# Kernel tuning notes

Measured on AMD Instinct MI355X. Metric: run time of the kernel, lower is better.

The kernel has to match this reference:

```python
import jax, jax.numpy as jnp
import numpy as np

B, P, G, E = 2, 16, 128, 96
C110, C011, C001 = 4, 2, 1
N, CO = 128, 2

def _pw(x, W, b):
    """1x1 conv of any spatial rank == pointwise channel mixing."""
    y = jnp.einsum('oc,bc...->bo...', W, x)
    return y + b.reshape((1, -1) + (1,) * (y.ndim - 2))

def _hidden(s110, s011, s001, Ws, bs):
    # s110:[B,C,P,G,1]  s011:[B,C,1,G,E]  s001:[B,C,1,1,E]
    # sub-stream order: [110 full, 110 pool-P, 110 pool-G, 011 full, 011 pool-G, 011 pool-E, 001]
    t110 = s110[..., 0]         # [B,C,P,G]
    t011 = s011[:, :, 0]        # [B,C,G,E]
    t001 = s001[:, :, 0, 0]     # [B,C,E]
    s = (_pw(t110, Ws[0], bs[0])[..., None]
         + _pw(t110.max(axis=2), Ws[1], bs[1])[:, :, None, :, None]
         + _pw(t110.max(axis=3), Ws[2], bs[2])[:, :, :, None, None]
         + _pw(t011, Ws[3], bs[3])[:, :, None, :, :]
         + _pw(t011.max(axis=2), Ws[4], bs[4])[:, :, None, None, :]
         + _pw(t011.max(axis=3), Ws[5], bs[5])[:, :, None, :, None]
         + _pw(t001, Ws[6], bs[6])[:, :, None, None, :])
    s = jax.nn.leaky_relu(s)    # [B,N,P,G,E]
    return (jnp.max(s, axis=4, keepdims=True),
            jnp.max(s, axis=2, keepdims=True),
            jnp.max(s, axis=(2, 3), keepdims=True))

def _forward(x110, x011, x001, W0_110, b0_110, W0_011, b0_011, W0_001, b0_001, W1, b1, Wact, bact, Wcrit, bcrit):
    Ws0 = [W0_110[0], W0_110[1], W0_110[2], W0_011[0], W0_011[1], W0_011[2], W0_001]
    bs0 = [b0_110[0], b0_110[1], b0_110[2], b0_011[0], b0_011[1], b0_011[2], b0_001]
    s110, s011, s001 = _hidden(x110, x011, x001, Ws0, bs0)
    s110, s011, s001 = _hidden(s110, s011, s001, list(W1), list(b1))
    t110 = s110[..., 0]  # [B,N,P,G]
    # actor head: eliminate G,E via mean pooling (dim_elimination_max_pooling=False)
    a110 = _pw(t110.mean(axis=3), Wact[0], bact[0])              # [B,CO,P]
    a011 = _pw(s011.mean(axis=(3, 4)), Wact[1], bact[1])         # [B,CO,1]
    a001 = _pw(s001[:, :, :, 0].mean(axis=3), Wact[2], bact[2])  # [B,CO,1]
    actions = jax.nn.leaky_relu(a110 + a011 + a001)              # [B,CO,P]
    # critic head: eliminate G via mean pooling
    c110 = _pw(t110.mean(axis=3), Wcrit[0], bcrit[0])            # [B,CO,P]
    c011 = _pw(s011[:, :, 0].mean(axis=2), Wcrit[1], bcrit[1])   # [B,CO,E]
    c001 = _pw(s001[:, :, 0, 0], Wcrit[2], bcrit[2])             # [B,CO,E]
    v = jax.nn.leaky_relu(c110[:, :, :, None] + (c011 + c001)[:, :, None, :])  # [B,CO,P,E]
    v110 = v.max(axis=3).sum(axis=2)  # stream (1,1,0): max over E, sum over P
    v011 = v.max(axis=2).sum(axis=2)  # streams (0,1,1) and (0,0,1) coincide numerically
    values = (2.0 + v110 + 2.0 * v011).reshape(-1)  # python sum(l, 2) starts at 2
    return actions, values

def setup_inputs() -> dict:
    key = jax.random.key(0)
    ks = jax.random.split(key, 12)
    f32 = jnp.float32
    def w(k, shape, fan):
        return jax.random.normal(k, shape, f32) / np.float32(np.sqrt(fan))
    return {
        'x110': jax.random.normal(ks[0], (B, C110, P, G, 1), f32),
        'x011': jax.random.normal(ks[1], (B, C011, 1, G, E), f32),
        'x001': jax.random.normal(ks[2], (B, C001, 1, 1, E), f32),
        'W0_110': w(ks[3], (3, N, C110), C110), 'b0_110': jnp.zeros((3, N), f32),
        'W0_011': w(ks[4], (3, N, C011), C011), 'b0_011': jnp.zeros((3, N), f32),
        'W0_001': w(ks[5], (N, C001), C001),    'b0_001': jnp.zeros((N,), f32),
        'W1':     w(ks[6], (7, N, N), N),       'b1':     jnp.zeros((7, N), f32),
        'Wact':   w(ks[7], (3, CO, N), N),      'bact':   jnp.zeros((3, CO), f32),
        'Wcrit':  w(ks[8], (3, CO, N), N),      'bcrit':  jnp.zeros((3, CO), f32),
    }

def reference(x110, x011, x001, W0_110, b0_110, W0_011, b0_011, W0_001, b0_001, W1, b1, Wact, bact, Wcrit, bcrit):
    return _forward(x110, x011, x001, W0_110, b0_110, W0_011, b0_011, W0_001, b0_001, W1, b1, Wact, bact, Wcrit, bcrit)
```

## Files before the change

### kernel.cpp

```cpp
#include <hip/hip_runtime.h>
#include <math.h>

#define DEVI __device__ __forceinline__

constexpr int B = 2, P = 16, G = 128, E = 96, N = 128, CO = 2;

DEVI float lrelu(float x) { return x > 0.f ? x : 0.01f * x; }

constexpr int OFF_U1     = 0;
constexpr int OFF_V1     = OFF_U1 + 524288;
constexpr int OFF_MAXPU0 = OFF_V1 + 3145728;
constexpr int OFF_MAXEV0 = OFF_MAXPU0 + 32768;
constexpr int OFF_MP110  = OFF_MAXEV0 + 32768;
constexpr int OFF_MG110  = OFF_MP110 + 32768;
constexpr int OFF_S001A  = OFF_MG110 + 4096;
constexpr int OFF_RMP    = OFF_S001A + 24576;
constexpr int OFF_RMG    = OFF_RMP + 1024;
constexpr int OFF_RME    = OFF_RMG + 128;
constexpr int OFF_RMG011 = OFF_RME + 512;
constexpr int OFF_C1P    = OFF_RMG011 + 384;
constexpr int OFF_BF1G   = OFF_C1P + 4096;
constexpr int OFF_EG1E   = OFF_BF1G + 32768;
constexpr int OFF_M110   = OFF_EG1E + 24576;
constexpr int OFF_M011E  = OFF_M110 + 4096;
constexpr int OFF_S001B  = OFF_M011E + 24576;

__global__ void __launch_bounds__(256) k_layer0(
    const float* __restrict__ x110, const float* __restrict__ x011,
    const float* __restrict__ x001,
    const float* __restrict__ W0_110, const float* __restrict__ b0_110,
    const float* __restrict__ W0_011, const float* __restrict__ b0_011,
    const float* __restrict__ W0_001, const float* __restrict__ b0_001,
    float* __restrict__ maxpU0g, float* __restrict__ maxeV0g,
    float* __restrict__ mp110, float* __restrict__ mg110,
    float* __restrict__ s001a,
    float* __restrict__ rmpG, float* __restrict__ rmgG,
    float* __restrict__ rmeG, float* __restrict__ rmg011G) {
  __shared__ float xs[4 * 16 * 128];
  __shared__ float v0[128 * 97];
  __shared__ float u0[16 * 128];
  __shared__ float rmp[4 * 128], rmgS[4 * 16], rme[2 * 128], rmg011L[2 * 96];
  __shared__ float mpu[128], mev[128], part[256];
  const int bn = blockIdx.x, b = bn >> 7, n = bn & 127, tid = threadIdx.x;

  {
    const float4* xsrc = (const float4*)(x110 + (size_t)b * 8192);
    float4* xdst = (float4*)xs;
#pragma unroll
    for (int k = 0; k < 8; k++) xdst[tid + k * 256] = xsrc[tid + k * 256];
  }
  __syncthreads();
  for (int i = tid; i < 512; i += 256) {
    int c = i >> 7, g = i & 127;
    float m = -INFINITY;
    for (int p = 0; p < P; p++) m = fmaxf(m, xs[(c * 16 + p) * 128 + g]);
    rmp[i] = m;
  }
  if (tid < 64) {
    int c = tid >> 4, p = tid & 15;
    float m = -INFINITY;
    for (int g = 0; g < G; g++) m = fmaxf(m, xs[(c * 16 + p) * 128 + g]);
    rmgS[tid] = m;
  }
  {
    int c = tid >> 7, g = tid & 127;
    const float4* r = (const float4*)(x011 + ((size_t)(b * 2 + c) * 128 + g) * 96);
    float m = -INFINITY;
#pragma unroll
    for (int j = 0; j < 24; j++) {
      float4 v = r[j];
      m = fmaxf(m, fmaxf(fmaxf(v.x, v.y), fmaxf(v.z, v.w)));
    }
    rme[tid] = m;
  }
  if (tid < 192) {
    int c = tid / 96, e = tid % 96;
    const float* pp = x011 + ((size_t)(b * 2 + c) * 128) * 96 + e;
    float m = -INFINITY;
    for (int g = 0; g < G; g++) m = fmaxf(m, pp[g * 96]);
    rmg011L[tid] = m;
  }
  __syncthreads();
  float w0[4], w1[4], w2[4];
#pragma unroll
  for (int cc = 0; cc < 4; cc++) {
    w0[cc] = W0_110[n * 4 + cc];
    w1[cc] = W0_110[512 + n * 4 + cc];
    w2[cc] = W0_110[1024 + n * 4 + cc];
  }
  float we0 = W0_011[512 + n * 2], we1 = W0_011[512 + n * 2 + 1];
  float bu = b0_110[n] + b0_110[128 + n] + b0_110[256 + n] + b0_011[256 + n];
  float vw00 = W0_011[n * 2], vw01 = W0_011[n * 2 + 1];
  float vw10 = W0_011[256 + n * 2], vw11 = W0_011[256 + n * 2 + 1];
  float w001 = W0_001[n];
  float bv = b0_011[n] + b0_011[128 + n] + b0_001[n];

#pragma unroll
  for (int k = 0; k < 8; k++) {
    int i = tid + k * 256, p = i >> 7, g = i & 127;
    float acc = bu + we0 * rme[g] + we1 * rme[128 + g];
#pragma unroll
    for (int cc = 0; cc < 4; cc++)
      acc += w0[cc] * xs[(cc * 16 + p) * 128 + g] + w1[cc] * rmp[cc * 128 + g]
           + w2[cc] * rmgS[cc * 16 + p];
    u0[i] = acc;
  }
  {
    const float* xa = x011 + (size_t)(b * 2) * 12288;
    const float* xb = xa + 12288;
    const float* xc = x001 + b * 96;
    for (int k = 0; k < 48; k++) {
      int i = tid + k * 256;
      int g = i / 96, e = i - g * 96;
      float val = bv + vw00 * xa[i] + vw01 * xb[i]
                + vw10 * rmg011L[e] + vw11 * rmg011L[96 + e] + w001 * xc[e];
      v0[g * 97 + e] = val;
    }
  }
  __syncthreads();
  if (tid < 128) {
    float m = -INFINITY;
    for (int p = 0; p < P; p++) m = fmaxf(m, u0[p * 128 + tid]);
    mpu[tid] = m;
    maxpU0g[bn * 128 + tid] = m;
  }
  {
    int g = tid & 127, h = tid >> 7;
    const float* r = &v0[g * 97 + h * 48];
    float m = -INFINITY;
    for (int j = 0; j < 48; j++) m = fmaxf(m, r[j]);
    part[tid] = m;
  }
  __syncthreads();
  if (tid < 128) {
    float m = fmaxf(part[tid], part[128 + tid]);
    mev[tid] = m;
    maxeV0g[bn * 128 + tid] = m;
    mp110[bn * 128 + tid] = lrelu(mpu[tid] + m);
  }
  __syncthreads();
  {
    int p = tid >> 4, ch = tid & 15;
    float m = -INFINITY;
    for (int g = ch * 8; g < ch * 8 + 8; g++)
      m = fmaxf(m, u0[p * 128 + g] + mev[g]);
    part[tid] = m;
  }
  if (tid < 96) {
    float m = -INFINITY;
    for (int g = 0; g < G; g++) m = fmaxf(m, mpu[g] + v0[g * 97 + tid]);
    s001a[bn * 96 + tid] = lrelu(m);
  }
  __syncthreads();
  if (tid < 16) {
    float m = -INFINITY;
    for (int ch = 0; ch < 16; ch++) m = fmaxf(m, part[tid * 16 + ch]);
    mg110[bn * 16 + tid] = lrelu(m);
  }
  if (n == 0) {
    for (int i = tid; i < 512; i += 256) rmpG[b * 512 + i] = rmp[i];
    if (tid < 64) rmgG[b * 64 + tid] = rmgS[tid];
    rmeG[b * 256 + tid] = rme[tid];
    if (tid < 192) rmg011G[b * 192 + tid] = rmg011L[tid];
  }
}

__global__ void k_sg(const float* __restrict__ W1, const float* __restrict__ mp110,
                     const float* __restrict__ mg110, const float* __restrict__ s001a,
                     float* __restrict__ C1p, float* __restrict__ BF1g,
                     float* __restrict__ EG1e) {
  int t = blockIdx.x * 256 + threadIdx.x;
  if (t < 4096) {
    int p = t & 15, n = (t >> 4) & 127, b = t >> 11;
    float acc = 0.f;
    for (int c = 0; c < N; c++)
      acc += W1[(2 * N + n) * N + c] * mg110[(b * N + c) * P + p];
    C1p[t] = acc;
  } else if (t < 36864) {
    int i = t - 4096;
    int g = i & 127, n = (i >> 7) & 127, b = i >> 14;
    float acc = 0.f;
    for (int c = 0; c < N; c++)
      acc += (W1[(1 * N + n) * N + c] + W1[(5 * N + n) * N + c])
             * mp110[(b * N + c) * G + g];
    BF1g[i] = acc;
  } else {
    int i = t - 36864;
    int e = i % 96; int r = i / 96; int n = r & 127, b = r >> 7;
    float acc = 0.f;
    for (int c = 0; c < N; c++)
      acc += (W1[(4 * N + n) * N + c] + W1[(6 * N + n) * N + c])
             * s001a[(b * N + c) * E + e];
    EG1e[i] = acc;
  }
}

__global__ void __launch_bounds__(256) k_layer1(
    const float* __restrict__ x110, const float* __restrict__ x011,
    const float* __restrict__ x001,
    const float* __restrict__ W0_110, const float* __restrict__ b0_110,
    const float* __restrict__ W0_011, const float* __restrict__ b0_011,
    const float* __restrict__ W0_001, const float* __restrict__ b0_001,
    const float* __restrict__ maxpU0g, const float* __restrict__ maxeV0g,
    const float* __restrict__ rmpG, const float* __restrict__ rmgG,
    const float* __restrict__ rmeG, const float* __restrict__ rmg011G,
    const float* __restrict__ W1, const float* __restrict__ b1,
    const float* __restrict__ C1p, const float* __restrict__ BF1g,
    const float* __restrict__ EG1e,
    float* __restrict__ U1, float* __restrict__ V1) {
  __shared__ float s110c[128 * 16];
  __shared__ float s011c[128 * 96];
  __shared__ float W0L110[1536], W0L011[768], W0L001[128];
  __shared__ float busum[128], bvsum[128], mpu[128], mev[128];
  __shared__ float x011row[192], rmg011s[192], x001s[96];
  __shared__ float x110col[64], rmg110p[64], rmp4[4], rme2[2];
  const int blk = blockIdx.x;
  const int b = blk >> 8, g = (blk >> 1) & 127, nh = blk & 1;
  const int n0 = nh * 64;
  const int tid = threadIdx.x;

  for (int i = tid; i < 1536; i += 256) W0L110[i] = W0_110[i];
  for (int i = tid; i < 768; i += 256) W0L011[i] = W0_011[i];
  if (tid < 128) {
    W0L001[tid] = W0_001[tid];
    busum[tid] = b0_110[tid] + b0_110[128 + tid] + b0_110[256 + tid] + b0_011[256 + tid];
    bvsum[tid] = b0_011[tid] + b0_011[128 + tid] + b0_001[tid];
    mpu[tid] = maxpU0g[(b * 128 + tid) * 128 + g];
    mev[tid] = maxeV0g[(b * 128 + tid) * 128 + g];
  }
  if (tid < 192) {
    int c = tid / 96, e = tid % 96;
    x011row[tid] = x011[((size_t)(b * 2 + c) * 128 + g) * 96 + e];
    rmg011s[tid] = rmg011G[b * 192 + tid];
  }
  if (tid < 96) x001s[tid] = x001[b * 96 + tid];
  if (tid < 64) {
    int c = tid >> 4, p = tid & 15;
    x110col[tid] = x110[((size_t)(b * 4 + c) * 16 + p) * 128 + g];
    rmg110p[tid] = rmgG[b * 64 + tid];
  }
  if (tid < 4) rmp4[tid] = rmpG[(b * 4 + tid) * 128 + g];
  if (tid < 2) rme2[tid] = rmeG[(b * 2 + tid) * 128 + g];
  __syncthreads();

#pragma unroll
  for (int k = 0; k < 8; k++) {
    int i = tid + k * 256, c = i >> 4, p = i & 15;
    float acc = busum[c] + W0L011[512 + c * 2] * rme2[0]
              + W0L011[512 + c * 2 + 1] * rme2[1];
#pragma unroll
    for (int cc = 0; cc < 4; cc++)
      acc += W0L110[c * 4 + cc] * x110col[cc * 16 + p]
           + W0L110[512 + c * 4 + cc] * rmp4[cc]
           + W0L110[1024 + c * 4 + cc] * rmg110p[cc * 16 + p];
    s110c[i] = lrelu(acc + mev[c]);
  }
  for (int k = 0; k < 48; k++) {
    int i = tid + k * 256;
    int c = i / 96, e = i - c * 96;
    float v = bvsum[c] + W0L011[c * 2] * x011row[e] + W0L011[c * 2 + 1] * x011row[96 + e]
            + W0L011[256 + c * 2] * rmg011s[e] + W0L011[256 + c * 2 + 1] * rmg011s[96 + e]
            + W0L001[c] * x001s[e];
    s011c[i] = lrelu(v + mpu[c]);
  }
  __syncthreads();

  {
    int nn = tid >> 2, pq = tid & 3;
    int n = n0 + nn;
    float bb = b1[n] + b1[128 + n] + b1[256 + n] + b1[640 + n]
             + BF1g[(b * 128 + n) * 128 + g];
    float4 cp = *(const float4*)&C1p[(b * 128 + n) * 16 + pq * 4];
    float4 a = make_float4(bb + cp.x, bb + cp.y, bb + cp.z, bb + cp.w);
    const float* wr = W1 + (size_t)n * 128;
    for (int c = 0; c < 128; c++) {
      float wv = wr[c];
      float4 s = *(const float4*)&s110c[c * 16 + pq * 4];
      a.x += wv * s.x; a.y += wv * s.y; a.z += wv * s.z; a.w += wv * s.w;
    }
    float* dst = U1 + ((size_t)(b * 128 + n) * 16 + pq * 4) * 128 + g;
    dst[0] = a.x; dst[128] = a.y; dst[256] = a.z; dst[384] = a.w;
  }
  {
    int n2 = tid >> 3, e0 = (tid & 7) * 12;
    int na = n0 + n2 * 2, nb = na + 1;
    float4 aA[3], aB[3];
    {
      float bbA = b1[384 + na] + b1[512 + na] + b1[768 + na];
      float bbB = b1[384 + nb] + b1[512 + nb] + b1[768 + nb];
      const float* egA = EG1e + (b * 128 + na) * 96 + e0;
      const float* egB = EG1e + (b * 128 + nb) * 96 + e0;
#pragma unroll
      for (int k = 0; k < 3; k++) {
        aA[k] = make_float4(bbA + egA[k * 4], bbA + egA[k * 4 + 1],
                            bbA + egA[k * 4 + 2], bbA + egA[k * 4 + 3]);
        aB[k] = make_float4(bbB + egB[k * 4], bbB + egB[k * 4 + 1],
                            bbB + egB[k * 4 + 2], bbB + egB[k * 4 + 3]);
      }
    }
    const float* wA = W1 + (size_t)(384 + na) * 128;
    const float* wB = W1 + (size_t)(384 + nb) * 128;
#pragma unroll 4
    for (int c = 0; c < 128; c++) {
      float4 s0 = *(const float4*)&s011c[c * 96 + e0];
      float4 s1 = *(const float4*)&s011c[c * 96 + e0 + 4];
      float4 s2 = *(const float4*)&s011c[c * 96 + e0 + 8];
      float wa = wA[c], wb = wB[c];
      aA[0].x += wa * s0.x; aA[0].y += wa * s0.y; aA[0].z += wa * s0.z; aA[0].w += wa * s0.w;
      aA[1].x += wa * s1.x; aA[1].y += wa * s1.y; aA[1].z += wa * s1.z; aA[1].w += wa * s1.w;
      aA[2].x += wa * s2.x; aA[2].y += wa * s2.y; aA[2].z += wa * s2.z; aA[2].w += wa * s2.w;
      aB[0].x += wb * s0.x; aB[0].y += wb * s0.y; aB[0].z += wb * s0.z; aB[0].w += wb * s0.w;
      aB[1].x += wb * s1.x; aB[1].y += wb * s1.y; aB[1].z += wb * s1.z; aB[1].w += wb * s1.w;
      aB[2].x += wb * s2.x; aB[2].y += wb * s2.y; aB[2].z += wb * s2.z; aB[2].w += wb * s2.w;
    }
    float* dA = V1 + ((size_t)(b * 128 + na) * 128 + g) * 96 + e0;
    float* dB = V1 + ((size_t)(b * 128 + nb) * 128 + g) * 96 + e0;
#pragma unroll
    for (int k = 0; k < 3; k++) {
      *(float4*)(dA + k * 4) = aA[k];
      *(float4*)(dB + k * 4) = aB[k];
    }
  }
}

__global__ void __launch_bounds__(256) k_post1(
    const float* __restrict__ U1, const float* __restrict__ V1,
    float* __restrict__ m110, float* __restrict__ m011e,
    float* __restrict__ s001b) {
  __shared__ float uU[P * G];
  __shared__ float part[256];
  __shared__ float smaxeV[G], smaxpU[G];
  const int bn = blockIdx.x;
  const int tid = threadIdx.x;
  const float4* usrc = (const float4*)(U1 + (size_t)bn * P * G);
  float4* udst = (float4*)uU;
  udst[tid] = usrc[tid];
  udst[tid + 256] = usrc[tid + 256];
  {
    int g = tid & 127, h = tid >> 7;
    const float* vrow = V1 + ((size_t)bn * G + g) * E + h * 48;
    float m = -INFINITY;
#pragma unroll
    for (int j = 0; j < 12; j++) {
      float4 v = *(const float4*)(vrow + j * 4);
      m = fmaxf(m, fmaxf(fmaxf(v.x, v.y), fmaxf(v.z, v.w)));
    }
    part[tid] = m;
  }
  __syncthreads();
  if (tid < G) {
    smaxeV[tid] = fmaxf(part[tid], part[tid + 128]);
    float mp = -INFINITY;
    for (int p = 0; p < P; p++) mp = fmaxf(mp, uU[p * G + tid]);
    smaxpU[tid] = mp;
  }
  __syncthreads();
  if (tid < P) {
    float s = 0.f;
    for (int g = 0; g < G; g++) s += lrelu(uU[tid * G + g] + smaxeV[g]);
    m110[bn * P + tid] = s * (1.f / G);
  }
  if (tid < E) {
    float s = 0.f, mm = -INFINITY;
    const float* vcol = V1 + (size_t)bn * G * E + tid;
    for (int g = 0; g < G; g++) {
      float pre = smaxpU[g] + vcol[g * E];
      s += lrelu(pre);
      mm = fmaxf(mm, pre);
    }
    m011e[bn * E + tid] = s * (1.f / G);
    s001b[bn * E + tid] = lrelu(mm);
  }
}

__global__ void __launch_bounds__(128) k_final(const float* __restrict__ m110,
                                               const float* __restrict__ m011e,
                                               const float* __restrict__ s001,
                                               const float* __restrict__ Wact,
                                               const float* __restrict__ bact,
                                               const float* __restrict__ Wcrit,
                                               const float* __restrict__ bcrit,
                                               float* __restrict__ out) {
  __shared__ float sm011[N], sm001[N], scp[P], sce[E], srow[P], scol[E];
  const int bo = blockIdx.x;
  const int o = bo & 1, b = bo >> 1;
  const int t = threadIdx.x;
  {
    float s1 = 0.f, s2 = 0.f;
    const float* p1 = m011e + (b * N + t) * E;
    const float* p2 = s001 + (b * N + t) * E;
    for (int e = 0; e < E; e++) { s1 += p1[e]; s2 += p2[e]; }
    sm011[t] = s1 * (1.f / E);
    sm001[t] = s2 * (1.f / E);
  }
  __syncthreads();
  if (t < P) {
    const float* wa0 = Wact + o * N;
    const float* wa1 = Wact + (1 * CO + o) * N;
    const float* wa2 = Wact + (2 * CO + o) * N;
    const float* wc0 = Wcrit + o * N;
    float a = 0.f, c = 0.f, aa = 0.f;
    for (int n = 0; n < N; n++) {
      float m = m110[(b * N + n) * P + t];
      a += wa0[n] * m;
      c += wc0[n] * m;
      aa += wa1[n] * sm011[n] + wa2[n] * sm001[n];
    }
    float act = a + aa + bact[o] + bact[CO + o] + bact[2 * CO + o];
    out[(b * CO + o) * P + t] = lrelu(act);
    scp[t] = c + bcrit[o];
  } else if (t < P + E) {
    int e = t - P;
    const float* wc1 = Wcrit + (1 * CO + o) * N;
    const float* wc2 = Wcrit + (2 * CO + o) * N;
    float c = 0.f;
    for (int n = 0; n < N; n++)
      c += wc1[n] * m011e[(b * N + n) * E + e] + wc2[n] * s001[(b * N + n) * E + e];
    sce[e] = c + bcrit[CO + o] + bcrit[2 * CO + o];
  }
  __syncthreads();
  if (t < P) {
    float m = -INFINITY;
    for (int e = 0; e < E; e++) m = fmaxf(m, lrelu(scp[t] + sce[e]));
    srow[t] = m;
  } else if (t < P + E) {
    int e = t - P;
    float m = -INFINITY;
    for (int p = 0; p < P; p++) m = fmaxf(m, lrelu(scp[p] + sce[e]));
    scol[e] = m;
  }
  __syncthreads();
  if (t == 0) {
    float v110 = 0.f, v011 = 0.f;
    for (int p = 0; p < P; p++) v110 += srow[p];
    for (int e = 0; e < E; e++) v011 += scol[e];
    out[B * CO * P + b * CO + o] = 2.f + v110 + 2.f * v011;
  }
}

extern "C" void kernel_launch(void* const* d_in, const int* in_sizes, int n_in,
                              void* d_out, int out_size, void* d_ws, size_t ws_size,
                              hipStream_t stream) {
  const float* x110   = (const float*)d_in[0];
  const float* x011   = (const float*)d_in[1];
  const float* x001   = (const float*)d_in[2];
  const float* W0_110 = (const float*)d_in[3];
  const float* b0_110 = (const float*)d_in[4];
  const float* W0_011 = (const float*)d_in[5];
  const float* b0_011 = (const float*)d_in[6];
  const float* W0_001 = (const float*)d_in[7];
  const float* b0_001 = (const float*)d_in[8];
  const float* W1     = (const float*)d_in[9];
  const float* b1     = (const float*)d_in[10];
  const float* Wact   = (const float*)d_in[11];
  const float* bact   = (const float*)d_in[12];
  const float* Wcrit  = (const float*)d_in[13];
  const float* bcrit  = (const float*)d_in[14];
  float* out = (float*)d_out;
  float* w = (float*)d_ws;

  float* U1     = w + OFF_U1;
  float* V1     = w + OFF_V1;
  float* maxpU0 = w + OFF_MAXPU0;
  float* maxeV0 = w + OFF_MAXEV0;
  float* mp110  = w + OFF_MP110;
  float* mg110  = w + OFF_MG110;
  float* s001a  = w + OFF_S001A;
  float* rmpG   = w + OFF_RMP;
  float* rmgG   = w + OFF_RMG;
  float* rmeG   = w + OFF_RME;
  float* rmg011 = w + OFF_RMG011;
  float* C1p    = w + OFF_C1P;
  float* BF1g   = w + OFF_BF1G;
  float* EG1e   = w + OFF_EG1E;
  float* m110   = w + OFF_M110;
  float* m011e  = w + OFF_M011E;
  float* s001b  = w + OFF_S001B;

  k_layer0<<<256, 256, 0, stream>>>(x110, x011, x001, W0_110, b0_110, W0_011,
                                    b0_011, W0_001, b0_001,
                                    maxpU0, maxeV0, mp110, mg110, s001a,
                                    rmpG, rmgG, rmeG, rmg011);
  k_sg<<<240, 256, 0, stream>>>(W1, mp110, mg110, s001a, C1p, BF1g, EG1e);
  k_layer1<<<512, 256, 0, stream>>>(x110, x011, x001, W0_110, b0_110, W0_011,
                                    b0_011, W0_001, b0_001,
                                    maxpU0, maxeV0, rmpG, rmgG, rmeG, rmg011,
                                    W1, b1, C1p, BF1g, EG1e, U1, V1);
  k_post1<<<256, 256, 0, stream>>>(U1, V1, m110, m011e, s001b);
  k_final<<<4, 128, 0, stream>>>(m110, m011e, s001b, Wact, bact, Wcrit, bcrit, out);
}
```

Baseline: 104.7 us.

## Fuse all five stages into one persistent kernel with atomic grid barriers

Replaces the five separate kernel launches with a single 256-block persistent kernel. Stages are separated by software grid barriers built on atomic counters, and the counters are reset by a memset before each launch. Shared memory is shared between stages through a union. The layer-1 stage is remapped so each block handles one (b,g) pair instead of the previous 512-block split, and the post stage now stages V1 into shared memory. The aim is to remove launch gaps and inter-kernel drain, at the cost of spin-wait barriers, a larger shared-memory footprint that may lower occupancy, and reliance on all 256 blocks being co-resident.

```diff
diff --git a/kernel.cpp b/kernel.cpp
--- a/kernel.cpp
+++ b/kernel.cpp
@@ -4,6 +4,7 @@
 #define DEVI __device__ __forceinline__
 
 constexpr int B = 2, P = 16, G = 128, E = 96, N = 128, CO = 2;
+constexpr int NBLK = 256;
 
 DEVI float lrelu(float x) { return x > 0.f ? x : 0.01f * x; }
 
@@ -24,417 +25,459 @@
 constexpr int OFF_M110   = OFF_EG1E + 24576;
 constexpr int OFF_M011E  = OFF_M110 + 4096;
 constexpr int OFF_S001B  = OFF_M011E + 24576;
-
-__global__ void __launch_bounds__(256) k_layer0(
+constexpr int OFF_CTR    = OFF_S001B + 24576;
+
+union alignas(16) SharedU {
+  struct {
+    float xs[4 * 16 * 128];
+    float v0[128 * 97];
+    float u0[16 * 128];
+    float rmp[512], rmgS[64], rme[256], rmg011L[192];
+    float mpu[128], mev[128], part[256];
+  } a;
+  struct {
+    float s110c[128 * 16];
+    float s011c[128 * 96];
+    float W0L110[1536], W0L011[768], W0L001[128];
+    float busum[128], bvsum[128], mpu[128], mev[128];
+    float x011row[192], rmg011s[192], x001s[96];
+    float x110col[64], rmg110p[64], rmp4[4], rme2[2];
+  } c;
+  struct {
+    float vrow[128 * 97];
+    float uU[16 * 128];
+    float part[256];
+    float smaxeV[128], smaxpU[128];
+  } d;
+  struct {
+    float sm011[128], sm001[128], scp[16], sce[96], srow[16], scol[96];
+  } e;
+};
+
+DEVI void grid_sync(unsigned* ctr) {
+  __syncthreads();
+  if (threadIdx.x == 0) {
+    __threadfence();
+    atomicAdd(ctr, 1u);
+    while (__hip_atomic_load(ctr, __ATOMIC_RELAXED, __HIP_MEMORY_SCOPE_AGENT)
+           < (unsigned)NBLK) {
+      __builtin_amdgcn_s_sleep(1);
+    }
+  }
+  __syncthreads();
+  __threadfence();
+}
+
+__global__ void __launch_bounds__(256) k_fused(
     const float* __restrict__ x110, const float* __restrict__ x011,
     const float* __restrict__ x001,
     const float* __restrict__ W0_110, const float* __restrict__ b0_110,
     const float* __restrict__ W0_011, const float* __restrict__ b0_011,
     const float* __restrict__ W0_001, const float* __restrict__ b0_001,
-    float* __restrict__ maxpU0g, float* __restrict__ maxeV0g,
-    float* __restrict__ mp110, float* __restrict__ mg110,
-    float* __restrict__ s001a,
-    float* __restrict__ rmpG, float* __restrict__ rmgG,
-    float* __restrict__ rmeG, float* __restrict__ rmg011G) {
-  __shared__ float xs[4 * 16 * 128];
-  __shared__ float v0[128 * 97];
-  __shared__ float u0[16 * 128];
-  __shared__ float rmp[4 * 128], rmgS[4 * 16], rme[2 * 128], rmg011L[2 * 96];
-  __shared__ float mpu[128], mev[128], part[256];
-  const int bn = blockIdx.x, b = bn >> 7, n = bn & 127, tid = threadIdx.x;
+    const float* __restrict__ W1, const float* __restrict__ b1,
+    const float* __restrict__ Wact, const float* __restrict__ bact,
+    const float* __restrict__ Wcrit, const float* __restrict__ bcrit,
+    float* __restrict__ out, float* __restrict__ w, unsigned* __restrict__ ctrs) {
+  __shared__ SharedU sh;
+  const int blk = blockIdx.x, tid = threadIdx.x;
+
+  float* U1      = w + OFF_U1;
+  float* V1      = w + OFF_V1;
+  float* maxpU0g = w + OFF_MAXPU0;
+  float* maxeV0g = w + OFF_MAXEV0;
+  float* mp110   = w + OFF_MP110;
+  float* mg110   = w + OFF_MG110;
+  float* s001a   = w + OFF_S001A;
+  float* rmpG    = w + OFF_RMP;
+  float* rmgG    = w + OFF_RMG;
+  float* rmeG    = w + OFF_RME;
+  float* rmg011G = w + OFF_RMG011;
+  float* C1p     = w + OFF_C1P;
+  float* BF1g    = w + OFF_BF1G;
+  float* EG1e    = w + OFF_EG1E;
+  float* m110    = w + OFF_M110;
+  float* m011e   = w + OFF_M011E;
+  float* s001b   = w + OFF_S001B;
 
   {
-    const float4* xsrc = (const float4*)(x110 + (size_t)b * 8192);
-    float4* xdst = (float4*)xs;
-#pragma unroll
-    for (int k = 0; k < 8; k++) xdst[tid + k * 256] = xsrc[tid + k * 256];
+    const int bn = blk, b = bn >> 7, n = bn & 127;
+    {
+      const float4* xsrc = (const float4*)(x110 + (size_t)b * 8192);
+      float4* xdst = (float4*)sh.a.xs;
+#pragma unroll
+      for (int k = 0; k < 8; k++) xdst[tid + k * 256] = xsrc[tid + k * 256];
+    }
+    __syncthreads();
+    for (int i = tid; i < 512; i += 256) {
+      int c = i >> 7, g = i & 127;
+      float m = -INFINITY;
+      for (int p = 0; p < P; p++) m = fmaxf(m, sh.a.xs[(c * 16 + p) * 128 + g]);
+      sh.a.rmp[i] = m;
+    }
+    if (tid < 64) {
+      int c = tid >> 4, p = tid & 15;
+      float m = -INFINITY;
+      for (int g = 0; g < G; g++) m = fmaxf(m, sh.a.xs[(c * 16 + p) * 128 + g]);
+      sh.a.rmgS[tid] = m;
+    }
+    {
+      int c = tid >> 7, g = tid & 127;
+      const float4* r = (const float4*)(x011 + ((size_t)(b * 2 + c) * 128 + g) * 96);
+      float m = -INFINITY;
+#pragma unroll
+      for (int j = 0; j < 24; j++) {
+        float4 v = r[j];
+        m = fmaxf(m, fmaxf(fmaxf(v.x, v.y), fmaxf(v.z, v.w)));
+      }
+      sh.a.rme[tid] = m;
+    }
+    if (tid < 192) {
+      int c = tid / 96, e = tid % 96;
+      const float* pp = x011 + ((size_t)(b * 2 + c) * 128) * 96 + e;
+      float m = -INFINITY;
+      for (int g = 0; g < G; g++) m = fmaxf(m, pp[g * 96]);
+      sh.a.rmg011L[tid] = m;
+    }
+    __syncthreads();
+    float w0[4], w1[4], w2[4];
+#pragma unroll
+    for (int cc = 0; cc < 4; cc++) {
+      w0[cc] = W0_110[n * 4 + cc];
+      w1[cc] = W0_110[512 + n * 4 + cc];
+      w2[cc] = W0_110[1024 + n * 4 + cc];
+    }
+    float we0 = W0_011[512 + n * 2], we1 = W0_011[512 + n * 2 + 1];
+    float bu = b0_110[n] + b0_110[128 + n] + b0_110[256 + n] + b0_011[256 + n];
+    float vw00 = W0_011[n * 2], vw01 = W0_011[n * 2 + 1];
+    float vw10 = W0_011[256 + n * 2], vw11 = W0_011[256 + n * 2 + 1];
+    float w001 = W0_001[n];
+    float bv = b0_011[n] + b0_011[128 + n] + b0_001[n];
+
+#pragma unroll
+    for (int k = 0; k < 8; k++) {
+      int i = tid + k * 256, p = i >> 7, g = i & 127;
+      float acc = bu + we0 * sh.a.rme[g] + we1 * sh.a.rme[128 + g];
+#pragma unroll
+      for (int cc = 0; cc < 4; cc++)
+        acc += w0[cc] * sh.a.xs[(cc * 16 + p) * 128 + g]
+             + w1[cc] * sh.a.rmp[cc * 128 + g]
+             + w2[cc] * sh.a.rmgS[cc * 16 + p];
+      sh.a.u0[i] = acc;
+    }
+    {
+      const float* xa = x011 + (size_t)(b * 2) * 12288;
+      const float* xb = xa + 12288;
+      const float* xc = x001 + b * 96;
+      for (int k = 0; k < 48; k++) {
+        int i = tid + k * 256;
+        int g = i / 96, e = i - g * 96;
+        float val = bv + vw00 * xa[i] + vw01 * xb[i]
+                  + vw10 * sh.a.rmg011L[e] + vw11 * sh.a.rmg011L[96 + e]
+                  + w001 * xc[e];
+        sh.a.v0[g * 97 + e] = val;
+      }
+    }
+    __syncthreads();
+    if (tid < 128) {
+      float m = -INFINITY;
+      for (int p = 0; p < P; p++) m = fmaxf(m, sh.a.u0[p * 128 + tid]);
+      sh.a.mpu[tid] = m;
+      maxpU0g[bn * 128 + tid] = m;
+    }
+    {
+      int g = tid & 127, h = tid >> 7;
+      const float* r = &sh.a.v0[g * 97 + h * 48];
+      float m = -INFINITY;
+      for (int j = 0; j < 48; j++) m = fmaxf(m, r[j]);
+      sh.a.part[tid] = m;
+    }
+    __syncthreads();
+    if (tid < 128) {
+      float m = fmaxf(sh.a.part[tid], sh.a.part[128 + tid]);
+      sh.a.mev[tid] = m;
+      maxeV0g[bn * 128 + tid] = m;
+      mp110[bn * 128 + tid] = lrelu(sh.a.mpu[tid] + m);
+    }
+    __syncthreads();
+    {
+      int p = tid >> 4, ch = tid & 15;
+      float m = -INFINITY;
+      for (int g = ch * 8; g < ch * 8 + 8; g++)
+        m = fmaxf(m, sh.a.u0[p * 128 + g] + sh.a.mev[g]);
+      sh.a.part[tid] = m;
+    }
+    if (tid < 96) {
+      float m = -INFINITY;
+      for (int g = 0; g < G; g++) m = fmaxf(m, sh.a.mpu[g] + sh.a.v0[g * 97 + tid]);
+      s001a[bn * 96 + tid] = lrelu(m);
+    }
+    __syncthreads();
+    if (tid < 16) {
+      float m = -INFINITY;
+      for (int ch = 0; ch < 16; ch++) m = fmaxf(m, sh.a.part[tid * 16 + ch]);
+      mg110[bn * 16 + tid] = lrelu(m);
+    }
+    if (n == 0) {
+      for (int i = tid; i < 512; i += 256) rmpG[b * 512 + i] = sh.a.rmp[i];
+      if (tid < 64) rmgG[b * 64 + tid] = sh.a.rmgS[tid];
+      rmeG[b * 256 + tid] = sh.a.rme[tid];
+      if (tid < 192) rmg011G[b * 192 + tid] = sh.a.rmg011L[tid];
+    }
   }
-  __syncthreads();
-  for (int i = tid; i < 512; i += 256) {
-    int c = i >> 7, g = i & 127;
-    float m = -INFINITY;
-    for (int p = 0; p < P; p++) m = fmaxf(m, xs[(c * 16 + p) * 128 + g]);
-    rmp[i] = m;
+  grid_sync(&ctrs[0]);
+
+  {
+    int t = blk * 256 + tid;
+    if (t < 4096) {
+      int p = t & 15, n = (t >> 4) & 127, b = t >> 11;
+      float acc = 0.f;
+      for (int c = 0; c < N; c++)
+        acc += W1[(2 * N + n) * N + c] * mg110[(b * N + c) * P + p];
+      C1p[t] = acc;
+    } else if (t < 36864) {
+      int i = t - 4096;
+      int g = i & 127, n = (i >> 7) & 127, b = i >> 14;
+      float acc = 0.f;
+      for (int c = 0; c < N; c++)
+        acc += (W1[(1 * N + n) * N + c] + W1[(5 * N + n) * N + c])
+               * mp110[(b * N + c) * G + g];
+      BF1g[i] = acc;
+    } else if (t < 61440) {
+      int i = t - 36864;
+      int e = i % 96; int r = i / 96; int n = r & 127, b = r >> 7;
+      float acc = 0.f;
+      for (int c = 0; c < N; c++)
+        acc += (W1[(4 * N + n) * N + c] + W1[(6 * N + n) * N + c])
+               * s001a[(b * N + c) * E + e];
+      EG1e[i] = acc;
+    }
   }
-  if (tid < 64) {
-    int c = tid >> 4, p = tid & 15;
-    float m = -INFINITY;
-    for (int g = 0; g < G; g++) m = fmaxf(m, xs[(c * 16 + p) * 128 + g]);
-    rmgS[tid] = m;
-  }
+  grid_sync(&ctrs[1]);
+
   {
-    int c = tid >> 7, g = tid & 127;
-    const float4* r = (const float4*)(x011 + ((size_t)(b * 2 + c) * 128 + g) * 96);
-    float m = -INFINITY;
-#pragma unroll
-    for (int j = 0; j < 24; j++) {
-      float4 v = r[j];
-      m = fmaxf(m, fmaxf(fmaxf(v.x, v.y), fmaxf(v.z, v.w)));
-    }
-    rme[tid] = m;
-  }
-  if (tid < 192) {
-    int c = tid / 96, e = tid % 96;
-    const float* pp = x011 + ((size_t)(b * 2 + c) * 128) * 96 + e;
-    float m = -INFINITY;
-    for (int g = 0; g < G; g++) m = fmaxf(m, pp[g * 96]);
-    rmg011L[tid] = m;
-  }
-  __syncthreads();
-  float w0[4], w1[4], w2[4];
-#pragma unroll
-  for (int cc = 0; cc < 4; cc++) {
-    w0[cc] = W0_110[n * 4 + cc];
-    w1[cc] = W0_110[512 + n * 4 + cc];
-    w2[cc] = W0_110[1024 + n * 4 + cc];
-  }
-  float we0 = W0_011[512 + n * 2], we1 = W0_011[512 + n * 2 + 1];
-  float bu = b0_110[n] + b0_110[128 + n] + b0_110[256 + n] + b0_011[256 + n];
-  float vw00 = W0_011[n * 2], vw01 = W0_011[n * 2 + 1];
-  float vw10 = W0_011[256 + n * 2], vw11 = W0_011[256 + n * 2 + 1];
-  float w001 = W0_001[n];
-  float bv = b0_011[n] + b0_011[128 + n] + b0_001[n];
-
-#pragma unroll
-  for (int k = 0; k < 8; k++) {
-    int i = tid + k * 256, p = i >> 7, g = i & 127;
-    float acc = bu + we0 * rme[g] + we1 * rme[128 + g];
-#pragma unroll
-    for (int cc = 0; cc < 4; cc++)
-      acc += w0[cc] * xs[(cc * 16 + p) * 128 + g] + w1[cc] * rmp[cc * 128 + g]
-           + w2[cc] * rmgS[cc * 16 + p];
-    u0[i] = acc;
-  }
-  {
-    const float* xa = x011 + (size_t)(b * 2) * 12288;
-    const float* xb = xa + 12288;
-    const float* xc = x001 + b * 96;
+    const int b = blk >> 7, g = blk & 127;
+    for (int i = tid; i < 1536; i += 256) sh.c.W0L110[i] = W0_110[i];
+    for (int i = tid; i < 768; i += 256) sh.c.W0L011[i] = W0_011[i];
+    if (tid < 128) {
+      sh.c.W0L001[tid] = W0_001[tid];
+      sh.c.busum[tid] = b0_110[tid] + b0_110[128 + tid] + b0_110[256 + tid]
+                      + b0_011[256 + tid];
+      sh.c.bvsum[tid] = b0_011[tid] + b0_011[128 + tid] + b0_001[tid];
+      sh.c.mpu[tid] = maxpU0g[(b * 128 + tid) * 128 + g];
+      sh.c.mev[tid] = maxeV0g[(b * 128 + tid) * 128 + g];
+    }
+    if (tid < 192) {
+      int c = tid / 96, e = tid % 96;
+      sh.c.x011row[tid] = x011[((size_t)(b * 2 + c) * 128 + g) * 96 + e];
+      sh.c.rmg011s[tid] = rmg011G[b * 192 + tid];
+    }
+    if (tid < 96) sh.c.x001s[tid] = x001[b * 96 + tid];
+    if (tid < 64) {
+      int c = tid >> 4, p = tid & 15;
+      sh.c.x110col[tid] = x110[((size_t)(b * 4 + c) * 16 + p) * 128 + g];
+      sh.c.rmg110p[tid] = rmgG[b * 64 + tid];
+    }
+    if (tid < 4) sh.c.rmp4[tid] = rmpG[(b * 4 + tid) * 128 + g];
+    if (tid < 2) sh.c.rme2[tid] = rmeG[(b * 2 + tid) * 128 + g];
+    __syncthreads();
+
+#pragma unroll
+    for (int k = 0; k < 8; k++) {
+      int i = tid + k * 256, c = i >> 4, p = i & 15;
+      float acc = sh.c.busum[c] + sh.c.W0L011[512 + c * 2] * sh.c.rme2[0]
+                + sh.c.W0L011[512 + c * 2 + 1] * sh.c.rme2[1];
+#pragma unroll
+      for (int cc = 0; cc < 4; cc++)
+        acc += sh.c.W0L110[c * 4 + cc] * sh.c.x110col[cc * 16 + p]
+             + sh.c.W0L110[512 + c * 4 + cc] * sh.c.rmp4[cc]
+             + sh.c.W0L110[1024 + c * 4 + cc] * sh.c.rmg110p[cc * 16 + p];
+      sh.c.s110c[i] = lrelu(acc + sh.c.mev[c]);
+    }
     for (int k = 0; k < 48; k++) {
       int i = tid + k * 256;
-      int g = i / 96, e = i - g * 96;
-      float val = bv + vw00 * xa[i] + vw01 * xb[i]
-                + vw10 * rmg011L[e] + vw11 * rmg011L[96 + e] + w001 * xc[e];
-      v0[g * 97 + e] = val;
+      int c = i / 96, e = i - c * 96;
+      float v = sh.c.bvsum[c]
+              + sh.c.W0L011[c * 2] * sh.c.x011row[e]
+              + sh.c.W0L011[c * 2 + 1] * sh.c.x011row[96 + e]
+              + sh.c.W0L011[256 + c * 2] * sh.c.rmg011s[e]
+              + sh.c.W0L011[256 + c * 2 + 1] * sh.c.rmg011s[96 + e]
+              + sh.c.W0L001[c] * sh.c.x001s[e];
+      sh.c.s011c[i] = lrelu(v + sh.c.mpu[c]);
+    }
+    __syncthreads();
+
+    {
+      int n = tid & 127, ph = tid >> 7;
+      float bb = b1[n] + b1[128 + n] + b1[256 + n] + b1[640 + n]
+               + BF1g[(b * 128 + n) * 128 + g];
+      const float* cp = &C1p[(b * 128 + n) * 16 + ph * 8];
+      float a[8];
+#pragma unroll
+      for (int j = 0; j < 8; j++) a[j] = bb + cp[j];
+      const float* wr = W1 + (size_t)n * 128;
+      for (int c = 0; c < 128; c++) {
+        float wv = wr[c];
+        float4 s0 = *(const float4*)&sh.c.s110c[c * 16 + ph * 8];
+        float4 s1 = *(const float4*)&sh.c.s110c[c * 16 + ph * 8 + 4];
+        a[0] += wv * s0.x; a[1] += wv * s0.y; a[2] += wv * s0.z; a[3] += wv * s0.w;
+        a[4] += wv * s1.x; a[5] += wv * s1.y; a[6] += wv * s1.z; a[7] += wv * s1.w;
+      }
+      float* dst = U1 + ((size_t)(b * 128 + n) * 16 + ph * 8) * 128 + g;
+#pragma unroll
+      for (int j = 0; j < 8; j++) dst[j * 128] = a[j];
+    }
+    {
+      int n0 = (tid >> 3) * 4, e0 = (tid & 7) * 12;
+      float4 acc[4][3];
+#pragma unroll
+      for (int ni = 0; ni < 4; ni++) {
+        int n = n0 + ni;
+        float bbv = b1[384 + n] + b1[512 + n] + b1[768 + n];
+        const float* eg = EG1e + (b * 128 + n) * 96 + e0;
+#pragma unroll
+        for (int k = 0; k < 3; k++)
+          acc[ni][k] = make_float4(bbv + eg[k * 4], bbv + eg[k * 4 + 1],
+                                   bbv + eg[k * 4 + 2], bbv + eg[k * 4 + 3]);
+      }
+      const float* wA = W1 + (size_t)(384 + n0) * 128;
+      for (int c = 0; c < 128; c += 4) {
+        float4 wv[4];
+#pragma unroll
+        for (int ni = 0; ni < 4; ni++)
+          wv[ni] = *(const float4*)&wA[ni * 128 + c];
+#pragma unroll
+        for (int cc = 0; cc < 4; cc++) {
+          float4 s0 = *(const float4*)&sh.c.s011c[(c + cc) * 96 + e0];
+          float4 s1 = *(const float4*)&sh.c.s011c[(c + cc) * 96 + e0 + 4];
+          float4 s2 = *(const float4*)&sh.c.s011c[(c + cc) * 96 + e0 + 8];
+#pragma unroll
+          for (int ni = 0; ni < 4; ni++) {
+            float wc = cc == 0 ? wv[ni].x : cc == 1 ? wv[ni].y
+                     : cc == 2 ? wv[ni].z : wv[ni].w;
+            acc[ni][0].x += wc * s0.x; acc[ni][0].y += wc * s0.y;
+            acc[ni][0].z += wc * s0.z; acc[ni][0].w += wc * s0.w;
+            acc[ni][1].x += wc * s1.x; acc[ni][1].y += wc * s1.y;
+            acc[ni][1].z += wc * s1.z; acc[ni][1].w += wc * s1.w;
+            acc[ni][2].x += wc * s2.x; acc[ni][2].y += wc * s2.y;
+            acc[ni][2].z += wc * s2.z; acc[ni][2].w += wc * s2.w;
+          }
+        }
+      }
+#pragma unroll
+      for (int ni = 0; ni < 4; ni++) {
+        float* dst = V1 + ((size_t)(b * 128 + n0 + ni) * 128 + g) * 96 + e0;
+#pragma unroll
+        for (int k = 0; k < 3; k++) *(float4*)(dst + k * 4) = acc[ni][k];
+      }
     }
   }
-  __syncthreads();
-  if (tid < 128) {
-    float m = -INFINITY;
-    for (int p = 0; p < P; p++) m = fmaxf(m, u0[p * 128 + tid]);
-    mpu[tid] = m;
-    maxpU0g[bn * 128 + tid] = m;
+  grid_sync(&ctrs[2]);
+
+  {
+    const int bn = blk;
+    const float4* usrc = (const float4*)(U1 + (size_t)bn * 2048);
+    ((float4*)sh.d.uU)[tid] = usrc[tid];
+    ((float4*)sh.d.uU)[tid + 256] = usrc[tid + 256];
+    const float4* vsrc = (const float4*)(V1 + (size_t)bn * 12288);
+#pragma unroll
+    for (int k = 0; k < 12; k++) {
+      int i4 = tid + k * 256;
+      float4 v = vsrc[i4];
+      int c = i4 / 24, e0 = (i4 - c * 24) * 4;
+      float* d = &sh.d.vrow[c * 97 + e0];
+      d[0] = v.x; d[1] = v.y; d[2] = v.z; d[3] = v.w;
+    }
+    __syncthreads();
+    {
+      int g = tid & 127, h = tid >> 7;
+      const float* r = &sh.d.vrow[g * 97 + h * 48];
+      float m = -INFINITY;
+      for (int j = 0; j < 48; j++) m = fmaxf(m, r[j]);
+      sh.d.part[tid] = m;
+    }
+    __syncthreads();
+    if (tid < 128) {
+      sh.d.smaxeV[tid] = fmaxf(sh.d.part[tid], sh.d.part[tid + 128]);
+      float mp = -INFINITY;
+      for (int p = 0; p < P; p++) mp = fmaxf(mp, sh.d.uU[p * 128 + tid]);
+      sh.d.smaxpU[tid] = mp;
+    }
+    __syncthreads();
+    if (tid >= 128 && tid < 144) {
+      int p = tid - 128;
+      float s = 0.f;
+      for (int g = 0; g < G; g++)
+        s += lrelu(sh.d.uU[p * 128 + g] + sh.d.smaxeV[g]);
+      m110[bn * 16 + p] = s * (1.f / G);
+    }
+    if (tid < 96) {
+      float s = 0.f, mm = -INFINITY;
+      for (int g = 0; g < G; g++) {
+        float pre = sh.d.smaxpU[g] + sh.d.vrow[g * 97 + tid];
+        s += lrelu(pre);
+        mm = fmaxf(mm, pre);
+      }
+      m011e[bn * 96 + tid] = s * (1.f / G);
+      s001b[bn * 96 + tid] = lrelu(mm);
+    }
   }
-  {
-    int g = tid & 127, h = tid >> 7;
-    const float* r = &v0[g * 97 + h * 48];
-    float m = -INFINITY;
-    for (int j = 0; j < 48; j++) m = fmaxf(m, r[j]);
-    part[tid] = m;
-  }
-  __syncthreads();
-  if (tid < 128) {
-    float m = fmaxf(part[tid], part[128 + tid]);
-    mev[tid] = m;
-    maxeV0g[bn * 128 + tid] = m;
-    mp110[bn * 128 + tid] = lrelu(mpu[tid] + m);
-  }
-  __syncthreads();
-  {
-    int p = tid >> 4, ch = tid & 15;
-    float m = -INFINITY;
-    for (int g = ch * 8; g < ch * 8 + 8; g++)
-      m = fmaxf(m, u0[p * 128 + g] + mev[g]);
-    part[tid] = m;
-  }
-  if (tid < 96) {
-    float m = -INFINITY;
-    for (int g = 0; g < G; g++) m = fmaxf(m, mpu[g] + v0[g * 97 + tid]);
-    s001a[bn * 96 + tid] = lrelu(m);
-  }
-  __syncthreads();
-  if (tid < 16) {
-    float m = -INFINITY;
-    for (int ch = 0; ch < 16; ch++) m = fmaxf(m, part[tid * 16 + ch]);
-    mg110[bn * 16 + tid] = lrelu(m);
-  }
-  if (n == 0) {
-    for (int i = tid; i < 512; i += 256) rmpG[b * 512 + i] = rmp[i];
-    if (tid < 64) rmgG[b * 64 + tid] = rmgS[tid];
-    rmeG[b * 256 + tid] = rme[tid];
-    if (tid < 192) rmg011G[b * 192 + tid] = rmg011L[tid];
-  }
-}
-
-__global__ void k_sg(const float* __restrict__ W1, const float* __restrict__ mp110,
-                     const float* __restrict__ mg110, const float* __restrict__ s001a,
-                     float* __restrict__ C1p, float* __restrict__ BF1g,
-                     float* __restrict__ EG1e) {
-  int t = blockIdx.x * 256 + threadIdx.x;
-  if (t < 4096) {
-    int p = t & 15, n = (t >> 4) & 127, b = t >> 11;
-    float acc = 0.f;
-    for (int c = 0; c < N; c++)
-      acc += W1[(2 * N + n) * N + c] * mg110[(b * N + c) * P + p];
-    C1p[t] = acc;
-  } else if (t < 36864) {
-    int i = t - 4096;
-    int g = i & 127, n = (i >> 7) & 127, b = i >> 14;
-    float acc = 0.f;
-    for (int c = 0; c < N; c++)
-      acc += (W1[(1 * N + n) * N + c] + W1[(5 * N + n) * N + c])
-             * mp110[(b * N + c) * G + g];
-    BF1g[i] = acc;
-  } else {
-    int i = t - 36864;
-    int e = i % 96; int r = i / 96; int n = r & 127, b = r >> 7;
-    float acc = 0.f;
-    for (int c = 0; c < N; c++)
-      acc += (W1[(4 * N + n) * N + c] + W1[(6 * N + n) * N + c])
-             * s001a[(b * N + c) * E + e];
-    EG1e[i] = acc;
-  }
-}
-
-__global__ void __launch_bounds__(256) k_layer1(
-    const float* __restrict__ x110, const float* __restrict__ x011,
-    const float* __restrict__ x001,
-    const float* __restrict__ W0_110, const float* __restrict__ b0_110,
-    const float* __restrict__ W0_011, const float* __restrict__ b0_011,
-    const float* __restrict__ W0_001, const float* __restrict__ b0_001,
-    const float* __restrict__ maxpU0g, const float* __restrict__ maxeV0g,
-    const float* __restrict__ rmpG, const float* __restrict__ rmgG,
-    const float* __restrict__ rmeG, const float* __restrict__ rmg011G,
-    const float* __restrict__ W1, const float* __restrict__ b1,
-    const float* __restrict__ C1p, const float* __restrict__ BF1g,
-    const float* __restrict__ EG1e,
-    float* __restrict__ U1, float* __restrict__ V1) {
-  __shared__ float s110c[128 * 16];
-  __shared__ float s011c[128 * 96];
-  __shared__ float W0L110[1536], W0L011[768], W0L001[128];
-  __shared__ float busum[128], bvsum[128], mpu[128], mev[128];
-  __shared__ float x011row[192], rmg011s[192], x001s[96];
-  __shared__ float x110col[64], rmg110p[64], rmp4[4], rme2[2];
-  const int blk = blockIdx.x;
-  const int b = blk >> 8, g = (blk >> 1) & 127, nh = blk & 1;
-  const int n0 = nh * 64;
-  const int tid = threadIdx.x;
-
-  for (int i = tid; i < 1536; i += 256) W0L110[i] = W0_110[i];
-  for (int i = tid; i < 768; i += 256) W0L011[i] = W0_011[i];
-  if (tid < 128) {
-    W0L001[tid] = W0_001[tid];
-    busum[tid] = b0_110[tid] + b0_110[128 + tid] + b0_110[256 + tid] + b0_011[256 + tid];
-    bvsum[tid] = b0_011[tid] + b0_011[128 + tid] + b0_001[tid];
-    mpu[tid] = maxpU0g[(b * 128 + tid) * 128 + g];
-    mev[tid] = maxeV0g[(b * 128 + tid) * 128 + g];
-  }
-  if (tid < 192) {
-    int c = tid / 96, e = tid % 96;
-    x011row[tid] = x011[((size_t)(b * 2 + c) * 128 + g) * 96 + e];
-    rmg011s[tid] = rmg011G[b * 192 + tid];
-  }
-  if (tid < 96) x001s[tid] = x001[b * 96 + tid];
-  if (tid < 64) {
-    int c = tid >> 4, p = tid & 15;
-    x110col[tid] = x110[((size_t)(b * 4 + c) * 16 + p) * 128 + g];
-    rmg110p[tid] = rmgG[b * 64 + tid];
-  }
-  if (tid < 4) rmp4[tid] = rmpG[(b * 4 + tid) * 128 + g];
-  if (tid < 2) rme2[tid] = rmeG[(b * 2 + tid) * 128 + g];
-  __syncthreads();
-
-#pragma unroll
-  for (int k = 0; k < 8; k++) {
-    int i = tid + k * 256, c = i >> 4, p = i & 15;
-    float acc = busum[c] + W0L011[512 + c * 2] * rme2[0]
-              + W0L011[512 + c * 2 + 1] * rme2[1];
-#pragma unroll
-    for (int cc = 0; cc < 4; cc++)
-      acc += W0L110[c * 4 + cc] * x110col[cc * 16 + p]
-           + W0L110[512 + c * 4 + cc] * rmp4[cc]
-           + W0L110[1024 + c * 4 + cc] * rmg110p[cc * 16 + p];
-    s110c[i] = lrelu(acc + mev[c]);
-  }
-  for (int k = 0; k < 48; k++) {
-    int i = tid + k * 256;
-    int c = i / 96, e = i - c * 96;
-    float v = bvsum[c] + W0L011[c * 2] * x011row[e] + W0L011[c * 2 + 1] * x011row[96 + e]
-            + W0L011[256 + c * 2] * rmg011s[e] + W0L011[256 + c * 2 + 1] * rmg011s[96 + e]
-            + W0L001[c] * x001s[e];
-    s011c[i] = lrelu(v + mpu[c]);
-  }
-  __syncthreads();
-
-  {
-    int nn = tid >> 2, pq = tid & 3;
-    int n = n0 + nn;
-    float bb = b1[n] + b1[128 + n] + b1[256 + n] + b1[640 + n]
-             + BF1g[(b * 128 + n) * 128 + g];
-    float4 cp = *(const float4*)&C1p[(b * 128 + n) * 16 + pq * 4];
-    float4 a = make_float4(bb + cp.x, bb + cp.y, bb + cp.z, bb + cp.w);
-    const float* wr = W1 + (size_t)n * 128;
-    for (int c = 0; c < 128; c++) {
-      float wv = wr[c];
-      float4 s = *(const float4*)&s110c[c * 16 + pq * 4];
-      a.x += wv * s.x; a.y += wv * s.y; a.z += wv * s.z; a.w += wv * s.w;
-    }
-    float* dst = U1 + ((size_t)(b * 128 + n) * 16 + pq * 4) * 128 + g;
-    dst[0] = a.x; dst[128] = a.y; dst[256] = a.z; dst[384] = a.w;
-  }
-  {
-    int n2 = tid >> 3, e0 = (tid & 7) * 12;
-    int na = n0 + n2 * 2, nb = na + 1;
-    float4 aA[3], aB[3];
-    {
-      float bbA = b1[384 + na] + b1[512 + na] + b1[768 + na];
-      float bbB = b1[384 + nb] + b1[512 + nb] + b1[768 + nb];
-      const float* egA = EG1e + (b * 128 + na) * 96 + e0;
-      const float* egB = EG1e + (b * 128 + nb) * 96 + e0;
-#pragma unroll
-      for (int k = 0; k < 3; k++) {
-        aA[k] = make_float4(bbA + egA[k * 4], bbA + egA[k * 4 + 1],
-                            bbA + egA[k * 4 + 2], bbA + egA[k * 4 + 3]);
-        aB[k] = make_float4(bbB + egB[k * 4], bbB + egB[k * 4 + 1],
-                            bbB + egB[k * 4 + 2], bbB + egB[k * 4 + 3]);
-      }
-    }
-    const float* wA = W1 + (size_t)(384 + na) * 128;
-    const float* wB = W1 + (size_t)(384 + nb) * 128;
-#pragma unroll 4
-    for (int c = 0; c < 128; c++) {
-      float4 s0 = *(const float4*)&s011c[c * 96 + e0];
-      float4 s1 = *(const float4*)&s011c[c * 96 + e0 + 4];
-      float4 s2 = *(const float4*)&s011c[c * 96 + e0 + 8];
-      float wa = wA[c], wb = wB[c];
-      aA[0].x += wa * s0.x; aA[0].y += wa * s0.y; aA[0].z += wa * s0.z; aA[0].w += wa * s0.w;
-      aA[1].x += wa * s1.x; aA[1].y += wa * s1.y; aA[1].z += wa * s1.z; aA[1].w += wa * s1.w;
-      aA[2].x += wa * s2.x; aA[2].y += wa * s2.y; aA[2].z += wa * s2.z; aA[2].w += wa * s2.w;
-      aB[0].x += wb * s0.x; aB[0].y += wb * s0.y; aB[0].z += wb * s0.z; aB[0].w += wb * s0.w;
-      aB[1].x += wb * s1.x; aB[1].y += wb * s1.y; aB[1].z += wb * s1.z; aB[1].w += wb * s1.w;
-      aB[2].x += wb * s2.x; aB[2].y += wb * s2.y; aB[2].z += wb * s2.z; aB[2].w += wb * s2.w;
-    }
-    float* dA = V1 + ((size_t)(b * 128 + na) * 128 + g) * 96 + e0;
-    float* dB = V1 + ((size_t)(b * 128 + nb) * 128 + g) * 96 + e0;
-#pragma unroll
-    for (int k = 0; k < 3; k++) {
-      *(float4*)(dA + k * 4) = aA[k];
-      *(float4*)(dB + k * 4) = aB[k];
-    }
-  }
-}
-
-__global__ void __launch_bounds__(256) k_post1(
-    const float* __restrict__ U1, const float* __restrict__ V1,
-    float* __restrict__ m110, float* __restrict__ m011e,
-    float* __restrict__ s001b) {
-  __shared__ float uU[P * G];
-  __shared__ float part[256];
-  __shared__ float smaxeV[G], smaxpU[G];
-  const int bn = blockIdx.x;
-  const int tid = threadIdx.x;
-  const float4* usrc = (const float4*)(U1 + (size_t)bn * P * G);
-  float4* udst = (float4*)uU;
-  udst[tid] = usrc[tid];
-  udst[tid + 256] = usrc[tid + 256];
-  {
-    int g = tid & 127, h = tid >> 7;
-    const float* vrow = V1 + ((size_t)bn * G + g) * E + h * 48;
-    float m = -INFINITY;
-#pragma unroll
-    for (int j = 0; j < 12; j++) {
-      float4 v = *(const float4*)(vrow + j * 4);
-      m = fmaxf(m, fmaxf(fmaxf(v.x, v.y), fmaxf(v.z, v.w)));
-    }
-    part[tid] = m;
-  }
-  __syncthreads();
-  if (tid < G) {
-    smaxeV[tid] = fmaxf(part[tid], part[tid + 128]);
-    float mp = -INFINITY;
-    for (int p = 0; p < P; p++) mp = fmaxf(mp, uU[p * G + tid]);
-    smaxpU[tid] = mp;
-  }
-  __syncthreads();
-  if (tid < P) {
-    float s = 0.f;
-    for (int g = 0; g < G; g++) s += lrelu(uU[tid * G + g] + smaxeV[g]);
-    m110[bn * P + tid] = s * (1.f / G);
-  }
-  if (tid < E) {
-    float s = 0.f, mm = -INFINITY;
-    const float* vcol = V1 + (size_t)bn * G * E + tid;
-    for (int g = 0; g < G; g++) {
-      float pre = smaxpU[g] + vcol[g * E];
-      s += lrelu(pre);
-      mm = fmaxf(mm, pre);
-    }
-    m011e[bn * E + tid] = s * (1.f / G);
-    s001b[bn * E + tid] = lrelu(mm);
-  }
-}
-
-__global__ void __launch_bounds__(128) k_final(const float* __restrict__ m110,
-                                               const float* __restrict__ m011e,
-                                               const float* __restrict__ s001,
-                                               const float* __restrict__ Wact,
-                                               const float* __restrict__ bact,
-                                               const float* __restrict__ Wcrit,
-                                               const float* __restrict__ bcrit,
-                                               float* __restrict__ out) {
-  __shared__ float sm011[N], sm001[N], scp[P], sce[E], srow[P], scol[E];
-  const int bo = blockIdx.x;
-  const int o = bo & 1, b = bo >> 1;
-  const int t = threadIdx.x;
-  {
-    float s1 = 0.f, s2 = 0.f;
-    const float* p1 = m011e + (b * N + t) * E;
-    const float* p2 = s001 + (b * N + t) * E;
-    for (int e = 0; e < E; e++) { s1 += p1[e]; s2 += p2[e]; }
-    sm011[t] = s1 * (1.f / E);
-    sm001[t] = s2 * (1.f / E);
-  }
-  __syncthreads();
-  if (t < P) {
-    const float* wa0 = Wact + o * N;
-    const float* wa1 = Wact + (1 * CO + o) * N;
-    const float* wa2 = Wact + (2 * CO + o) * N;
-    const float* wc0 = Wcrit + o * N;
-    float a = 0.f, c = 0.f, aa = 0.f;
-    for (int n = 0; n < N; n++) {
-      float m = m110[(b * N + n) * P + t];
-      a += wa0[n] * m;
-      c += wc0[n] * m;
-      aa += wa1[n] * sm011[n] + wa2[n] * sm001[n];
-    }
-    float act = a + aa + bact[o] + bact[CO + o] + bact[2 * CO + o];
-    out[(b * CO + o) * P + t] = lrelu(act);
-    scp[t] = c + bcrit[o];
-  } else if (t < P + E) {
-    int e = t - P;
-    const float* wc1 = Wcrit + (1 * CO + o) * N;
-    const float* wc2 = Wcrit + (2 * CO + o) * N;
-    float c = 0.f;
-    for (int n = 0; n < N; n++)
-      c += wc1[n] * m011e[(b * N + n) * E + e] + wc2[n] * s001[(b * N + n) * E + e];
-    sce[e] = c + bcrit[CO + o] + bcrit[2 * CO + o];
-  }
-  __syncthreads();
-  if (t < P) {
-    float m = -INFINITY;
-    for (int e = 0; e < E; e++) m = fmaxf(m, lrelu(scp[t] + sce[e]));
-    srow[t] = m;
-  } else if (t < P + E) {
-    int e = t - P;
-    float m = -INFINITY;
-    for (int p = 0; p < P; p++) m = fmaxf(m, lrelu(scp[p] + sce[e]));
-    scol[e] = m;
-  }
-  __syncthreads();
-  if (t == 0) {
-    float v110 = 0.f, v011 = 0.f;
-    for (int p = 0; p < P; p++) v110 += srow[p];
-    for (int e = 0; e < E; e++) v011 += scol[e];
-    out[B * CO * P + b * CO + o] = 2.f + v110 + 2.f * v011;
+  grid_sync(&ctrs[3]);
+
+  if (blk < 4) {
+    const int o = blk & 1, b = blk >> 1;
+    const int t = tid;
+    if (t < 128) {
+      float s1 = 0.f, s2 = 0.f;
+      const float* p1 = m011e + (b * N + t) * E;
+      const float* p2 = s001b + (b * N + t) * E;
+      for (int e = 0; e < E; e++) { s1 += p1[e]; s2 += p2[e]; }
+      sh.e.sm011[t] = s1 * (1.f / E);
+      sh.e.sm001[t] = s2 * (1.f / E);
+    }
+    __syncthreads();
+    if (t < P) {
+      const float* wa0 = Wact + o * N;
+      const float* wa1 = Wact + (1 * CO + o) * N;
+      const float* wa2 = Wact + (2 * CO + o) * N;
+      const float* wc0 = Wcrit + o * N;
+      float a = 0.f, c = 0.f, aa = 0.f;
+      for (int n = 0; n < N; n++) {
+        float m = m110[(b * N + n) * P + t];
+        a += wa0[n] * m;
+        c += wc0[n] * m;
+        aa += wa1[n] * sh.e.sm011[n] + wa2[n] * sh.e.sm001[n];
+      }
+      float act = a + aa + bact[o] + bact[CO + o] + bact[2 * CO + o];
+      out[(b * CO + o) * P + t] = lrelu(act);
+      sh.e.scp[t] = c + bcrit[o];
+    } else if (t < P + E) {
+      int e = t - P;
+      const float* wc1 = Wcrit + (1 * CO + o) * N;
+      const float* wc2 = Wcrit + (2 * CO + o) * N;
+      float c = 0.f;
+      for (int n = 0; n < N; n++)
+        c += wc1[n] * m011e[(b * N + n) * E + e]
+           + wc2[n] * s001b[(b * N + n) * E + e];
+      sh.e.sce[e] = c + bcrit[CO + o] + bcrit[2 * CO + o];
+    }
+    __syncthreads();
+    if (t < P) {
+      float m = -INFINITY;
+      for (int e = 0; e < E; e++) m = fmaxf(m, lrelu(sh.e.scp[t] + sh.e.sce[e]));
+      sh.e.srow[t] = m;
+    } else if (t < P + E) {
+      int e = t - P;
+      float m = -INFINITY;
+      for (int p = 0; p < P; p++) m = fmaxf(m, lrelu(sh.e.scp[p] + sh.e.sce[e]));
+      sh.e.scol[e] = m;
+    }
+    __syncthreads();
+    if (t == 0) {
+      float v110 = 0.f, v011 = 0.f;
+      for (int p = 0; p < P; p++) v110 += sh.e.srow[p];
+      for (int e = 0; e < E; e++) v011 += sh.e.scol[e];
+      out[B * CO * P + b * CO + o] = 2.f + v110 + 2.f * v011;
+    }
   }
 }
 
@@ -458,34 +501,10 @@
   const float* bcrit  = (const float*)d_in[14];
   float* out = (float*)d_out;
   float* w = (float*)d_ws;
-
-  float* U1     = w + OFF_U1;
-  float* V1     = w + OFF_V1;
-  float* maxpU0 = w + OFF_MAXPU0;
-  float* maxeV0 = w + OFF_MAXEV0;
-  float* mp110  = w + OFF_MP110;
-  float* mg110  = w + OFF_MG110;
-  float* s001a  = w + OFF_S001A;
-  float* rmpG   = w + OFF_RMP;
-  float* rmgG   = w + OFF_RMG;
-  float* rmeG   = w + OFF_RME;
-  float* rmg011 = w + OFF_RMG011;
-  float* C1p    = w + OFF_C1P;
-  float* BF1g   = w + OFF_BF1G;
-  float* EG1e   = w + OFF_EG1E;
-  float* m110   = w + OFF_M110;
-  float* m011e  = w + OFF_M011E;
-  float* s001b  = w + OFF_S001B;
-
-  k_layer0<<<256, 256, 0, stream>>>(x110, x011, x001, W0_110, b0_110, W0_011,
-                                    b0_011, W0_001, b0_001,
-                                    maxpU0, maxeV0, mp110, mg110, s001a,
-                                    rmpG, rmgG, rmeG, rmg011);
-  k_sg<<<240, 256, 0, stream>>>(W1, mp110, mg110, s001a, C1p, BF1g, EG1e);
-  k_layer1<<<512, 256, 0, stream>>>(x110, x011, x001, W0_110, b0_110, W0_011,
-                                    b0_011, W0_001, b0_001,
-                                    maxpU0, maxeV0, rmpG, rmgG, rmeG, rmg011,
-                                    W1, b1, C1p, BF1g, EG1e, U1, V1);
-  k_post1<<<256, 256, 0, stream>>>(U1, V1, m110, m011e, s001b);
-  k_final<<<4, 128, 0, stream>>>(m110, m011e, s001b, Wact, bact, Wcrit, bcrit, out);
+  unsigned* ctrs = (unsigned*)(w + OFF_CTR);
+
+  hipMemsetAsync(ctrs, 0, 4 * sizeof(unsigned), stream);
+  k_fused<<<NBLK, 256, 0, stream>>>(x110, x011, x001, W0_110, b0_110, W0_011,
+                                    b0_011, W0_001, b0_001, W1, b1,
+                                    Wact, bact, Wcrit, bcrit, out, w, ctrs);
 }
```

Measured after the change: 226.2 us. 116% more time.
